# Kernel tuning notes

Hardware: AMD Instinct MI355X
Metric: run time of the kernel (lower is better)

## Reference

```python
import jax, jax.numpy as jnp
import numpy as np
from jax import lax

W = 50      # window size
EPS = 1e-5  # BatchNorm eps (torch default)


def setup_inputs() -> dict:
    key = jax.random.key(0)
    ks = jax.random.split(key, 40)
    def n(i, shape, s=0.1):
        return (jax.random.normal(ks[i], shape, dtype=jnp.float32) * s).astype(jnp.float32)
    inp = {}
    inp['x'] = jax.random.normal(ks[0], (16, 1, 2048), dtype=jnp.float32)
    # conv stack (eval-mode BatchNorm: running mean/var are params)
    inp['conv1_w'] = n(1, (64, 1, 9));  inp['conv1_b'] = n(2, (64,))
    inp['bn1_g'] = 1.0 + n(3, (64,));   inp['bn1_b'] = n(4, (64,))
    inp['bn1_m'] = n(5, (64,));         inp['bn1_v'] = 0.5 + jax.random.uniform(ks[6], (64,), dtype=jnp.float32)
    inp['conv2_w'] = n(7, (32, 64, 7)); inp['conv2_b'] = n(8, (32,))
    inp['bn2_g'] = 1.0 + n(9, (32,));   inp['bn2_b'] = n(10, (32,))
    inp['bn2_m'] = n(11, (32,));        inp['bn2_v'] = 0.5 + jax.random.uniform(ks[12], (32,), dtype=jnp.float32)
    inp['conv3_w'] = n(13, (16, 32, 5)); inp['conv3_b'] = n(14, (16,))
    inp['bn3_g'] = 1.0 + n(15, (16,));   inp['bn3_b'] = n(16, (16,))
    inp['bn3_m'] = n(17, (16,));         inp['bn3_v'] = 0.5 + jax.random.uniform(ks[18], (16,), dtype=jnp.float32)
    # 2-layer LSTM, hidden 64, input 16 (torch gate order i,f,g,o)
    H = 64
    inp['wih0'] = n(19, (4 * H, 16)); inp['whh0'] = n(20, (4 * H, H))
    inp['bih0'] = n(21, (4 * H,));    inp['bhh0'] = n(22, (4 * H,))
    inp['wih1'] = n(23, (4 * H, H));  inp['whh1'] = n(24, (4 * H, H))
    inp['bih1'] = n(25, (4 * H,));    inp['bhh1'] = n(26, (4 * H,))
    # classifier 64 -> 32 -> 2
    inp['fc1_w'] = n(27, (32, H)); inp['fc1_b'] = n(28, (32,))
    inp['fc2_w'] = n(29, (2, 32)); inp['fc2_b'] = n(30, (2,))
    return inp


def _conv1d(x, w, b, pad):
    # x: [N, Cin, L], w: [Cout, Cin, K]
    y = lax.conv_general_dilated(x, w, (1,), [(pad, pad)],
                                 dimension_numbers=('NCH', 'OIH', 'NCH'))
    return y + b[:, None]


def _bn(x, g, b, m, v):
    # eval-mode BatchNorm1d over channel dim of [N, C, L]
    return (x - m[:, None]) * (g / jnp.sqrt(v + EPS))[:, None] + b[:, None]


def _lstm_layer(x, wih, whh, bih, bhh):
    # x: [B, T, D] -> [B, T, H]; torch gate order (i, f, g, o)
    B, T, D = x.shape
    H = whh.shape[1]
    xs = jnp.transpose(x, (1, 0, 2))                     # [T, B, D]
    pre = xs @ wih.T + (bih + bhh)                       # [T, B, 4H] input projection, hoisted
    def step(carry, p):
        h, c = carry
        g = p + h @ whh.T
        i, f, gg, o = jnp.split(g, 4, axis=-1)
        c = jax.nn.sigmoid(f) * c + jax.nn.sigmoid(i) * jnp.tanh(gg)
        h = jax.nn.sigmoid(o) * jnp.tanh(c)
        return (h, c), h
    h0 = jnp.zeros((B, H), x.dtype)
    _, hs = lax.scan(step, (h0, h0), pre)
    return jnp.transpose(hs, (1, 0, 2))


def reference(x, conv1_w, conv1_b, bn1_g, bn1_b, bn1_m, bn1_v,
              conv2_w, conv2_b, bn2_g, bn2_b, bn2_m, bn2_v,
              conv3_w, conv3_b, bn3_g, bn3_b, bn3_m, bn3_v,
              wih0, whh0, bih0, bhh0, wih1, whh1, bih1, bhh1,
              fc1_w, fc1_b, fc2_w, fc2_b):
    B, C, T = x.shape
    # sliding windows with left zero-pad of W-1 -> [B, T, C, W]
    xp = jnp.pad(x, ((0, 0), (0, 0), (W - 1, 0)))
    idx = jnp.arange(T)[:, None] + jnp.arange(W)[None, :]  # [T, W]
    win = xp[:, :, idx]                                    # [B, C, T, W]
    win = jnp.transpose(win, (0, 2, 1, 3)).reshape(B * T, C, W)
    # conv -> BN(eval) -> ReLU stack (dropout is identity in eval)
    h = jax.nn.relu(_bn(_conv1d(win, conv1_w, conv1_b, 4), bn1_g, bn1_b, bn1_m, bn1_v))
    h = jax.nn.relu(_bn(_conv1d(h, conv2_w, conv2_b, 3), bn2_g, bn2_b, bn2_m, bn2_v))
    h = jax.nn.relu(_bn(_conv1d(h, conv3_w, conv3_b, 2), bn3_g, bn3_b, bn3_m, bn3_v))
    feats = h.mean(axis=-1).reshape(B, T, -1)              # AdaptiveAvgPool1d(1) -> [B, T, 16]
    # 2-layer LSTM
    h1 = _lstm_layer(feats, wih0, whh0, bih0, bhh0)
    h2 = _lstm_layer(h1, wih1, whh1, bih1, bhh1)           # [B, T, 64]
    # classifier
    z = jax.nn.relu(h2 @ fc1_w.T + fc1_b)
    logits = z @ fc2_w.T + fc2_b                           # [B, T, 2]
    return logits
```

## Files before the change

kernel.cpp:

```cpp
#include <hip/hip_runtime.h>

#define EPSV 1e-5f
#define SCOPE_AGENT __HIP_MEMORY_SCOPE_AGENT

__device__ __forceinline__ float fast_rcp(float x) { return __builtin_amdgcn_rcpf(x); }
__device__ __forceinline__ float tanhfast(float x) {
    float e = __expf(2.0f * x);
    return 1.0f - 2.0f * fast_rcp(e + 1.0f);
}
__device__ __forceinline__ float dot4(const float4 w, const float4 v, float a) {
    a = fmaf(w.x, v.x, a);
    a = fmaf(w.y, v.y, a);
    a = fmaf(w.z, v.z, a);
    a = fmaf(w.w, v.w, a);
    return a;
}
#define DPPF(v, ctrl) __int_as_float(__builtin_amdgcn_mov_dpp(__float_as_int(v), (ctrl), 0xF, 0xF, false))

typedef unsigned long long ull;

struct RecS {
    float hbuf[2][80];
    float ring[16][64];
    float xst[16][80];
};
struct EdgeS {
    float A1[64 * 40];
    float A2[32 * 32];
    float xeL[24], xeR[24];
    float s1[64], t1[64], s2[32], t2[32], s3[16], t3[16];
    float psumE[288];
    float pi[512];
};

__global__ void pack_kernel(const float* __restrict__ w2, const float* __restrict__ w3,
                            float* __restrict__ w2t2, float4* __restrict__ w3p4,
                            float* __restrict__ w3p1, int* __restrict__ sync_ints) {
    int j = blockIdx.x * 256 + threadIdx.x;
    if (j < 16384) {
        int i = j >> 8;
        int o = (j >> 3) & 31;
        int k = j & 7;
        w2t2[j] = (k < 7) ? w2[o * 448 + i * 7 + k] : 0.0f;
    } else if (j < 16896) {
        int e = j - 16384;
        int i = e >> 4, o = e & 15;
        int base = o * 160 + i * 5;
        w3p4[e] = make_float4(w3[base], w3[base + 1], w3[base + 2], w3[base + 3]);
        w3p1[e] = w3[base + 4];
    } else if (j < 16896 + 4096) {
        sync_ints[j - 16896] = 0;
    }
}

__global__ __launch_bounds__(256) void conv1f_kernel(
    const float* __restrict__ x, const float* __restrict__ w1,
    const float* __restrict__ b1, const float* __restrict__ g1,
    const float* __restrict__ be1, const float* __restrict__ m1,
    const float* __restrict__ vv1, float* __restrict__ a1f)
{
    __shared__ float xs[72];
    const int tid = threadIdx.x;
    const int T = blockIdx.x * 64;
    const int b = blockIdx.y;
    if (tid < 72) {
        int gi = T - 49 + tid;
        xs[tid] = (gi >= 0 && gi < 2048) ? x[b * 2048 + gi] : 0.0f;
    }
    const int i = tid & 63, q = tid >> 6;
    float wv[9];
    #pragma unroll
    for (int k = 0; k < 9; ++k) wv[k] = w1[i * 9 + k];
    float sc = g1[i] * rsqrtf(vv1[i] + EPSV);
    float tc = (b1[i] - m1[i]) * sc + be1[i];
    __syncthreads();
    #pragma unroll
    for (int r = 0; r < 16; ++r) {
        int v1 = T + q * 16 + r;
        if (v1 < 2089) {
            float acc = 0.0f;
            #pragma unroll
            for (int k = 0; k < 9; ++k) acc = fmaf(wv[k], xs[q * 16 + r + k], acc);
            a1f[((long)b * 2089 + v1) * 64 + i] = fmaxf(acc * sc + tc, 0.0f);
        }
    }
}

__global__ __launch_bounds__(256) void conv2f_kernel(
    const float* __restrict__ a1f, const float* __restrict__ w2t2,
    const float* __restrict__ b2, const float* __restrict__ g2,
    const float* __restrict__ be2, const float* __restrict__ m2,
    const float* __restrict__ vv2, float* __restrict__ a2f)
{
    __shared__ __align__(16) float As[64 * 104];
    const int tid = threadIdx.x;
    const int T = blockIdx.x * 64;
    const int b = blockIdx.y;
    for (int idx = tid; idx < 1120; idx += 256) {
        int j = idx >> 4, i4 = (idx & 15) * 4;
        int v1 = T + j; if (v1 > 2088) v1 = 2088;
        float4 f = *(const float4*)&a1f[((long)b * 2089 + v1) * 64 + i4];
        int sj = j + ((j >> 3) << 2);
        As[(i4 + 0) * 104 + sj] = f.x;
        As[(i4 + 1) * 104 + sj] = f.y;
        As[(i4 + 2) * 104 + sj] = f.z;
        As[(i4 + 3) * 104 + sj] = f.w;
    }
    const int o = tid >> 3, pg = tid & 7;
    float sc = g2[o] * rsqrtf(vv2[o] + EPSV);
    float tc = (b2[o] - m2[o]) * sc + be2[o];
    __syncthreads();
    float acc[8];
    #pragma unroll
    for (int q = 0; q < 8; ++q) acc[q] = 0.0f;
    for (int i = 0; i < 64; ++i) {
        const float* rowp = &As[i * 104 + 12 * pg];
        float4 A0 = *(const float4*)&rowp[0];
        float4 A1 = *(const float4*)&rowp[4];
        float4 A2 = *(const float4*)&rowp[12];
        float2 A3 = *(const float2*)&rowp[16];
        const float4* wp = (const float4*)&w2t2[(i * 32 + o) * 8];
        float4 Wa = wp[0], Wb = wp[1];
        float av[14] = {A0.x, A0.y, A0.z, A0.w, A1.x, A1.y, A1.z, A1.w,
                        A2.x, A2.y, A2.z, A2.w, A3.x, A3.y};
        float wk[7] = {Wa.x, Wa.y, Wa.z, Wa.w, Wb.x, Wb.y, Wb.z};
        #pragma unroll
        for (int k = 0; k < 7; ++k) {
            #pragma unroll
            for (int q = 0; q < 8; ++q) acc[q] = fmaf(wk[k], av[q + k], acc[q]);
        }
    }
    #pragma unroll
    for (int q = 0; q < 8; ++q) {
        int v2 = T + pg * 8 + q;
        if (v2 < 2083)
            a2f[((long)b * 2083 + v2) * 32 + o] = fmaxf(acc[q] * sc + tc, 0.0f);
    }
}

__global__ __launch_bounds__(256) void conv3f_kernel(
    const float* __restrict__ a2f,
    const float4* __restrict__ w3p4, const float* __restrict__ w3p1,
    const float* __restrict__ b3, const float* __restrict__ g3,
    const float* __restrict__ be3, const float* __restrict__ m3,
    const float* __restrict__ vv3, float* __restrict__ a3f)
{
    __shared__ __align__(16) float A2s[32 * 200];
    const int tid = threadIdx.x;
    const int T = blockIdx.x * 128;
    const int b = blockIdx.y;
    for (int idx = tid; idx < 1056; idx += 256) {
        int j = idx >> 3, i4 = (idx & 7) * 4;
        int v2 = T + j; if (v2 > 2082) v2 = 2082;
        float4 f = *(const float4*)&a2f[((long)b * 2083 + v2) * 32 + i4];
        int sj = j + ((j >> 3) << 2);
        A2s[(i4 + 0) * 200 + sj] = f.x;
        A2s[(i4 + 1) * 200 + sj] = f.y;
        A2s[(i4 + 2) * 200 + sj] = f.z;
        A2s[(i4 + 3) * 200 + sj] = f.w;
    }
    const int o = tid & 15, pg = tid >> 4;
    float sc = g3[o] * rsqrtf(vv3[o] + EPSV);
    float tc = (b3[o] - m3[o]) * sc + be3[o];
    __syncthreads();
    float acc[8];
    #pragma unroll
    for (int q = 0; q < 8; ++q) acc[q] = 0.0f;
    for (int i = 0; i < 32; ++i) {
        const float* rowp = &A2s[i * 200 + 12 * pg];
        float4 R0 = *(const float4*)&rowp[0];
        float4 R1 = *(const float4*)&rowp[4];
        float4 R2 = *(const float4*)&rowp[12];
        float av[12] = {R0.x, R0.y, R0.z, R0.w, R1.x, R1.y, R1.z, R1.w,
                        R2.x, R2.y, R2.z, R2.w};
        float4 wa = w3p4[i * 16 + o];
        float w4 = w3p1[i * 16 + o];
        #pragma unroll
        for (int q = 0; q < 8; ++q) {
            acc[q] = fmaf(wa.x, av[q], acc[q]);
            acc[q] = fmaf(wa.y, av[q + 1], acc[q]);
            acc[q] = fmaf(wa.z, av[q + 2], acc[q]);
            acc[q] = fmaf(wa.w, av[q + 3], acc[q]);
            acc[q] = fmaf(w4,   av[q + 4], acc[q]);
        }
    }
    #pragma unroll
    for (int q = 0; q < 8; ++q) {
        int v3 = T + pg * 8 + q;
        if (v3 < 2079)
            a3f[((long)b * 2080 + v3) * 16 + o] = fmaxf(acc[q] * sc + tc, 0.0f);
        else if (v3 < 2080)
            a3f[((long)b * 2080 + v3) * 16 + o] = 0.0f;
    }
}

__device__ __forceinline__ void rec0_body(char* smemraw, int b,
    const float* __restrict__ feats,
    const float* __restrict__ wih, const float* __restrict__ whh,
    const float* __restrict__ bih, const float* __restrict__ bhh,
    float* __restrict__ hout, int* __restrict__ cnt0, int* __restrict__ flag1)
{
    RecS* s = (RecS*)smemraw;
    const int tid = threadIdx.x;
    const int j = tid >> 2, kq = tid & 3;

    const float4* pa = (const float4*)(whh + (0 * 64 + j) * 64 + kq * 16);
    const float4* pb = (const float4*)(whh + (1 * 64 + j) * 64 + kq * 16);
    const float4* pc_ = (const float4*)(whh + (2 * 64 + j) * 64 + kq * 16);
    const float4* pd = (const float4*)(whh + (3 * 64 + j) * 64 + kq * 16);
    float4 A0 = pa[0], A1 = pa[1], A2 = pa[2], A3 = pa[3];
    float4 B0 = pb[0], B1 = pb[1], B2 = pb[2], B3 = pb[3];
    float4 C0 = pc_[0], C1 = pc_[1], C2 = pc_[2], C3 = pc_[3];
    float4 D0 = pd[0], D1 = pd[1], D2 = pd[2], D3 = pd[3];
    float4 xw0 = *(const float4*)(wih + (0 * 64 + j) * 16 + kq * 4);
    float4 xw1 = *(const float4*)(wih + (1 * 64 + j) * 16 + kq * 4);
    float4 xw2 = *(const float4*)(wih + (2 * 64 + j) * 16 + kq * 4);
    float4 xw3 = *(const float4*)(wih + (3 * 64 + j) * 16 + kq * 4);
    const float bb0 = bih[j] + bhh[j];
    const float bb1 = bih[64 + j] + bhh[64 + j];
    const float bb2 = bih[128 + j] + bhh[128 + j];
    const float bb3 = bih[192 + j] + bhh[192 + j];

    if (tid < 64) s->hbuf[1][(tid >> 4) * 20 + (tid & 15)] = 0.0f;
    float cst = 0.0f;
    const float* fbase = feats + (long)b * 32768;
    __syncthreads();

#define STEP0(k) { \
        const float4* hp_ = (const float4*)&s->hbuf[((k) + 1) & 1][kq * 20]; \
        float4 h0_ = hp_[0], h1_ = hp_[1], h2_ = hp_[2], h3_ = hp_[3]; \
        float4 xv_ = *(const float4*)&s->xst[(k)][kq * 4]; \
        float p0 = dot4(A3, h3_, dot4(A2, h2_, dot4(A1, h1_, dot4(A0, h0_, dot4(xw0, xv_, 0.f))))); \
        float p1 = dot4(B3, h3_, dot4(B2, h2_, dot4(B1, h1_, dot4(B0, h0_, dot4(xw1, xv_, 0.f))))); \
        float p2 = dot4(C3, h3_, dot4(C2, h2_, dot4(C1, h1_, dot4(C0, h0_, dot4(xw2, xv_, 0.f))))); \
        float p3 = dot4(D3, h3_, dot4(D2, h2_, dot4(D1, h1_, dot4(D0, h0_, dot4(xw3, xv_, 0.f))))); \
        p0 += DPPF(p0, 0xB1); p1 += DPPF(p1, 0xB1); p2 += DPPF(p2, 0xB1); p3 += DPPF(p3, 0xB1); \
        p0 += DPPF(p0, 0x4E); p1 += DPPF(p1, 0x4E); p2 += DPPF(p2, 0x4E); p3 += DPPF(p3, 0x4E); \
        float gi = 1.0f - fast_rcp(__expf(p0 + bb0) + 1.0f); \
        float gf = 1.0f - fast_rcp(__expf(p1 + bb1) + 1.0f); \
        float gg = 1.0f - 2.0f * fast_rcp(__expf(2.0f * (p2 + bb2)) + 1.0f); \
        float go = 1.0f - fast_rcp(__expf(p3 + bb3) + 1.0f); \
        cst = fmaf(gf, cst, gi * gg); \
        float h_ = go * tanhfast(cst); \
        if (kq == 0) { s->hbuf[(k) & 1][(j >> 4) * 20 + (j & 15)] = h_; s->ring[(k)][j] = h_; } \
        __syncthreads(); \
    }

    for (int c = 0; c < 128; ++c) {
        if (tid == 0) {
            while (__hip_atomic_load(&cnt0[b * 128 + c], __ATOMIC_RELAXED, SCOPE_AGENT) < 16)
                __builtin_amdgcn_s_sleep(2);
        }
        __syncthreads();
        s->xst[tid >> 4][tid & 15] =
            __hip_atomic_load(fbase + c * 256 + tid, __ATOMIC_RELAXED, SCOPE_AGENT);
        __syncthreads();
        STEP0(0)  STEP0(1)  STEP0(2)  STEP0(3)
        STEP0(4)  STEP0(5)  STEP0(6)  STEP0(7)
        STEP0(8)  STEP0(9)  STEP0(10) STEP0(11)
        STEP0(12) STEP0(13) STEP0(14) STEP0(15)
        {
            ull* dst = (ull*)(hout + ((long)b * 2048 + c * 16) * 64);
            ull v0 = ((const ull*)s->ring)[tid];
            ull v1 = ((const ull*)s->ring)[tid + 256];
            __hip_atomic_store(dst + tid, v0, __ATOMIC_RELAXED, SCOPE_AGENT);
            __hip_atomic_store(dst + tid + 256, v1, __ATOMIC_RELAXED, SCOPE_AGENT);
            __syncthreads();
            if (tid == 0)
                __hip_atomic_store(&flag1[b * 128 + c], 1, __ATOMIC_RELAXED, SCOPE_AGENT);
        }
    }
#undef STEP0
}

__device__ __forceinline__ void rec1_body(char* smemraw, int b,
    const float* __restrict__ h1o,
    const float* __restrict__ wih, const float* __restrict__ whh,
    const float* __restrict__ bih, const float* __restrict__ bhh,
    float* __restrict__ hout, int* __restrict__ flag1)
{
    RecS* s = (RecS*)smemraw;
    const int tid = threadIdx.x;
    const int j = tid >> 2, kq = tid & 3;

    const float4* pa = (const float4*)(whh + (0 * 64 + j) * 64 + kq * 16);
    const float4* pb = (const float4*)(whh + (1 * 64 + j) * 64 + kq * 16);
    const float4* pc_ = (const float4*)(whh + (2 * 64 + j) * 64 + kq * 16);
    const float4* pd = (const float4*)(whh + (3 * 64 + j) * 64 + kq * 16);
    float4 A0 = pa[0], A1 = pa[1], A2 = pa[2], A3 = pa[3];
    float4 B0 = pb[0], B1 = pb[1], B2 = pb[2], B3 = pb[3];
    float4 C0 = pc_[0], C1 = pc_[1], C2 = pc_[2], C3 = pc_[3];
    float4 D0 = pd[0], D1 = pd[1], D2 = pd[2], D3 = pd[3];
    const float4* qa = (const float4*)(wih + (0 * 64 + j) * 64 + kq * 16);
    const float4* qb = (const float4*)(wih + (1 * 64 + j) * 64 + kq * 16);
    const float4* qc = (const float4*)(wih + (2 * 64 + j) * 64 + kq * 16);
    const float4* qd = (const float4*)(wih + (3 * 64 + j) * 64 + kq * 16);
    float4 XA0 = qa[0], XA1 = qa[1], XA2 = qa[2], XA3 = qa[3];
    float4 XB0 = qb[0], XB1 = qb[1], XB2 = qb[2], XB3 = qb[3];
    float4 XC0 = qc[0], XC1 = qc[1], XC2 = qc[2], XC3 = qc[3];
    float4 XD0 = qd[0], XD1 = qd[1], XD2 = qd[2], XD3 = qd[3];
    const float bb0 = bih[j] + bhh[j];
    const float bb1 = bih[64 + j] + bhh[64 + j];
    const float bb2 = bih[128 + j] + bhh[128 + j];
    const float bb3 = bih[192 + j] + bhh[192 + j];

    if (tid < 64) s->hbuf[1][(tid >> 4) * 20 + (tid & 15)] = 0.0f;
    float cst = 0.0f;
    __syncthreads();

#define STEP1(k) { \
        const float4* hp_ = (const float4*)&s->hbuf[((k) + 1) & 1][kq * 20]; \
        float4 h0_ = hp_[0], h1_ = hp_[1], h2_ = hp_[2], h3_ = hp_[3]; \
        const float4* xp_ = (const float4*)&s->xst[(k)][kq * 20]; \
        float4 x0_ = xp_[0], x1_ = xp_[1], x2_ = xp_[2], x3_ = xp_[3]; \
        float p0 = dot4(A3, h3_, dot4(A2, h2_, dot4(A1, h1_, dot4(A0, h0_, \
                   dot4(XA3, x3_, dot4(XA2, x2_, dot4(XA1, x1_, dot4(XA0, x0_, 0.f)))))))); \
        float p1 = dot4(B3, h3_, dot4(B2, h2_, dot4(B1, h1_, dot4(B0, h0_, \
                   dot4(XB3, x3_, dot4(XB2, x2_, dot4(XB1, x1_, dot4(XB0, x0_, 0.f)))))))); \
        float p2 = dot4(C3, h3_, dot4(C2, h2_, dot4(C1, h1_, dot4(C0, h0_, \
                   dot4(XC3, x3_, dot4(XC2, x2_, dot4(XC1, x1_, dot4(XC0, x0_, 0.f)))))))); \
        float p3 = dot4(D3, h3_, dot4(D2, h2_, dot4(D1, h1_, dot4(D0, h0_, \
                   dot4(XD3, x3_, dot4(XD2, x2_, dot4(XD1, x1_, dot4(XD0, x0_, 0.f)))))))); \
        p0 += DPPF(p0, 0xB1); p1 += DPPF(p1, 0xB1); p2 += DPPF(p2, 0xB1); p3 += DPPF(p3, 0xB1); \
        p0 += DPPF(p0, 0x4E); p1 += DPPF(p1, 0x4E); p2 += DPPF(p2, 0x4E); p3 += DPPF(p3, 0x4E); \
        float gi = 1.0f - fast_rcp(__expf(p0 + bb0) + 1.0f); \
        float gf = 1.0f - fast_rcp(__expf(p1 + bb1) + 1.0f); \
        float gg = 1.0f - 2.0f * fast_rcp(__expf(2.0f * (p2 + bb2)) + 1.0f); \
        float go = 1.0f - fast_rcp(__expf(p3 + bb3) + 1.0f); \
        cst = fmaf(gf, cst, gi * gg); \
        float h_ = go * tanhfast(cst); \
        if (kq == 0) { s->hbuf[(k) & 1][(j >> 4) * 20 + (j & 15)] = h_; s->ring[(k)][j] = h_; } \
        __syncthreads(); \
    }

    for (int c = 0; c < 128; ++c) {
        if (tid == 0) {
            while (__hip_atomic_load(&flag1[b * 128 + c], __ATOMIC_RELAXED, SCOPE_AGENT) < 1)
                __builtin_amdgcn_s_sleep(2);
        }
        __syncthreads();
        {
            const ull* src = (const ull*)(h1o + ((long)b * 2048 + c * 16) * 64);
            ull v0 = __hip_atomic_load(src + tid, __ATOMIC_RELAXED, SCOPE_AGENT);
            ull v1 = __hip_atomic_load(src + tid + 256, __ATOMIC_RELAXED, SCOPE_AGENT);
            int u0 = tid, u1 = tid + 256;
            int k0 = u0 >> 5, p0i = (u0 & 31) * 2;
            int k1 = u1 >> 5, p1i = (u1 & 31) * 2;
            *(ull*)&s->xst[k0][(p0i >> 4) * 20 + (p0i & 15)] = v0;
            *(ull*)&s->xst[k1][(p1i >> 4) * 20 + (p1i & 15)] = v1;
        }
        __syncthreads();
        STEP1(0)  STEP1(1)  STEP1(2)  STEP1(3)
        STEP1(4)  STEP1(5)  STEP1(6)  STEP1(7)
        STEP1(8)  STEP1(9)  STEP1(10) STEP1(11)
        STEP1(12) STEP1(13) STEP1(14) STEP1(15)
        {
            float4* dst = (float4*)(hout + ((long)b * 2048 + c * 16) * 64);
            dst[tid] = ((const float4*)s->ring)[tid];
        }
    }
#undef STEP1
}

__device__ __forceinline__ void edge_body(char* smemraw, int b, int t,
    const float* __restrict__ x,
    const float* __restrict__ w1,
    const float* __restrict__ b1, const float* __restrict__ g1,
    const float* __restrict__ be1, const float* __restrict__ m1, const float* __restrict__ vv1,
    const float* __restrict__ b2, const float* __restrict__ g2,
    const float* __restrict__ be2, const float* __restrict__ m2, const float* __restrict__ vv2,
    const float* __restrict__ b3, const float* __restrict__ g3,
    const float* __restrict__ be3, const float* __restrict__ m3, const float* __restrict__ vv3,
    const float* __restrict__ w2t2,
    const float4* __restrict__ w3p4, const float* __restrict__ w3p1,
    const float* __restrict__ a3f,
    float* __restrict__ feats, int* __restrict__ cnt0)
{
    EdgeS* s = (EdgeS*)smemraw;
    const int tid = threadIdx.x;

    if (tid < 128) {
        int dv = tid >> 2, o4 = (tid & 3) * 4;
        *(float4*)&s->pi[dv * 16 + o4] =
            *(const float4*)&a3f[((long)b * 2080 + t + dv) * 16 + o4];
    }
    if (tid < 64) {
        float sc = g1[tid] * rsqrtf(vv1[tid] + EPSV);
        s->s1[tid] = sc;
        s->t1[tid] = (b1[tid] - m1[tid]) * sc + be1[tid];
    } else if (tid < 96) {
        int o = tid - 64;
        float sc = g2[o] * rsqrtf(vv2[o] + EPSV);
        s->s2[o] = sc;
        s->t2[o] = (b2[o] - m2[o]) * sc + be2[o];
    } else if (tid < 112) {
        int o = tid - 96;
        float sc = g3[o] * rsqrtf(vv3[o] + EPSV);
        s->s3[o] = sc;
        s->t3[o] = (b3[o] - m3[o]) * sc + be3[o];
    } else if (tid < 136) {
        int j = tid - 112;
        float v = 0.0f;
        if (j >= 4 && j < 22) { int gi = t - 53 + j; if (gi >= 0) v = x[b * 2048 + gi]; }
        s->xeL[j] = v;
    } else if (tid < 160) {
        int j = tid - 136;
        float v = 0.0f;
        if (j <= 17) { int gi = t - 17 + j; if (gi >= 0) v = x[b * 2048 + gi]; }
        s->xeR[j] = v;
    }
    for (int idx = tid; idx < 384; idx += 256) {
        int o = idx / 6, z = idx - o * 6;
        s->A1[o * 40 + (z < 3 ? z : 31 + z)] = 0.0f;
    }
    if (tid < 128) {
        int o = tid >> 2, z = tid & 3;
        s->A2[o * 32 + (z < 2 ? z : 25 + z)] = 0.0f;
    }
    __syncthreads();

    {
        int o = tid >> 2, g = tid & 3;
        float wv[9];
        #pragma unroll
        for (int k = 0; k < 9; ++k) wv[k] = w1[o * 9 + k];
        float sc = s->s1[o], tc = s->t1[o];
        #pragma unroll
        for (int n = 0; n < 7; ++n) {
            int P = g * 7 + n;
            float acc = 0.0f;
            if (P < 14) {
                #pragma unroll
                for (int k = 0; k < 9; ++k) acc = fmaf(wv[k], s->xeL[P + k], acc);
                s->A1[o * 40 + 3 + P] = fmaxf(acc * sc + tc, 0.0f);
            } else {
                int pr = P - 14;
                #pragma unroll
                for (int k = 0; k < 9; ++k) acc = fmaf(wv[k], s->xeR[pr + k], acc);
                s->A1[o * 40 + 20 + pr] = fmaxf(acc * sc + tc, 0.0f);
            }
        }
    }
    __syncthreads();

    {
        int o = tid >> 3, g = tid & 7;
        int side = g >> 2, gg = g & 3;
        int be_ = gg * 3;
        int cnt = (gg == 3) ? 2 : 3;
        int beta0 = side ? 20 + be_ : be_;
        float acc0 = 0.f, acc1 = 0.f, acc2 = 0.f;
        for (int i = 0; i < 64; ++i) {
            const float* rp = &s->A1[i * 40 + beta0];
            float av[9];
            #pragma unroll
            for (int c = 0; c < 9; ++c) av[c] = rp[c];
            const float4* wp = (const float4*)&w2t2[(i * 32 + o) * 8];
            float4 Wa = wp[0], Wb = wp[1];
            float wk[7] = {Wa.x, Wa.y, Wa.z, Wa.w, Wb.x, Wb.y, Wb.z};
            #pragma unroll
            for (int k = 0; k < 7; ++k) {
                acc0 = fmaf(wk[k], av[k], acc0);
                acc1 = fmaf(wk[k], av[k + 1], acc1);
                acc2 = fmaf(wk[k], av[k + 2], acc2);
            }
        }
        float sc = s->s2[o], tc = s->t2[o];
        float r0 = fmaxf(acc0 * sc + tc, 0.0f);
        float r1 = fmaxf(acc1 * sc + tc, 0.0f);
        float r2 = fmaxf(acc2 * sc + tc, 0.0f);
        int base = o * 32 + (side ? 16 + be_ : 2 + be_);
        s->A2[base] = r0;
        s->A2[base + 1] = r1;
        if (cnt == 3) s->A2[base + 2] = r2;
    }
    __syncthreads();

    {
        int o = tid & 15, g = tid >> 4;
        float sc = s->s3[o], tc = s->t3[o];
        #pragma unroll
        for (int rep = 0; rep < 2; ++rep) {
            int P3 = (rep == 0) ? g : 16 + g;
            if (rep == 1 && g >= 2) break;
            int tb = (P3 >= 9) ? 16 + (P3 - 9) : P3;
            float acc = 0.0f;
            for (int i = 0; i < 32; ++i) {
                const float* rp = &s->A2[i * 32 + tb];
                float4 wa = w3p4[i * 16 + o];
                float w4 = w3p1[i * 16 + o];
                acc = fmaf(wa.x, rp[0], acc);
                acc = fmaf(wa.y, rp[1], acc);
                acc = fmaf(wa.z, rp[2], acc);
                acc = fmaf(wa.w, rp[3], acc);
                acc = fmaf(w4,   rp[4], acc);
            }
            s->psumE[P3 * 16 + o] = fmaxf(acc * sc + tc, 0.0f);
        }
    }
    __syncthreads();

    if (tid < 16) {
        float e = 0.0f;
        #pragma unroll
        for (int P3 = 0; P3 < 18; ++P3) e += s->psumE[P3 * 16 + tid];
        float ii = 0.0f;
        #pragma unroll
        for (int dv = 0; dv < 32; ++dv) ii += s->pi[dv * 16 + tid];
        __hip_atomic_store(&feats[((long)b * 2048 + t) * 16 + tid], (e + ii) * (1.0f / 50.0f),
                           __ATOMIC_RELAXED, SCOPE_AGENT);
    }
    __syncthreads();
    if (tid == 0)
        __hip_atomic_fetch_add(&cnt0[b * 128 + (t >> 4)], 1, __ATOMIC_RELAXED, SCOPE_AGENT);
}

__global__ __launch_bounds__(256, 2) void fused_kernel(
    const float* __restrict__ x,
    const float* __restrict__ w1, const float* __restrict__ b1,
    const float* __restrict__ g1, const float* __restrict__ be1,
    const float* __restrict__ m1, const float* __restrict__ vv1,
    const float* __restrict__ b2,
    const float* __restrict__ g2, const float* __restrict__ be2,
    const float* __restrict__ m2, const float* __restrict__ vv2,
    const float* __restrict__ b3,
    const float* __restrict__ g3, const float* __restrict__ be3,
    const float* __restrict__ m3, const float* __restrict__ vv3,
    const float* __restrict__ w2t2,
    const float4* __restrict__ w3p4, const float* __restrict__ w3p1,
    const float* __restrict__ a3f,
    const float* __restrict__ wih0, const float* __restrict__ whh0,
    const float* __restrict__ bih0, const float* __restrict__ bhh0,
    const float* __restrict__ wih1, const float* __restrict__ whh1,
    const float* __restrict__ bih1, const float* __restrict__ bhh1,
    float* __restrict__ feats, float* __restrict__ h1o, float* __restrict__ h2o,
    int* __restrict__ cnt0, int* __restrict__ flag1)
{
    __shared__ __align__(16) char smem[sizeof(EdgeS) > sizeof(RecS) ? sizeof(EdgeS) : sizeof(RecS)];

    if (blockIdx.x < 16) { rec0_body(smem, blockIdx.x, feats, wih0, whh0, bih0, bhh0, h1o, cnt0, flag1); return; }
    if (blockIdx.x < 32) { rec1_body(smem, blockIdx.x - 16, h1o, wih1, whh1, bih1, bhh1, h2o, flag1); return; }

    int w = blockIdx.x - 32;
    int b = w & 15;
    int t = w >> 4;
    edge_body(smem, b, t, x, w1, b1, g1, be1, m1, vv1, b2, g2, be2, m2, vv2,
              b3, g3, be3, m3, vv3, w2t2, w3p4, w3p1, a3f, feats, cnt0);
}

__global__ __launch_bounds__(256) void fc_kernel(
    const float* __restrict__ h2o,
    const float* __restrict__ fc1w, const float* __restrict__ fc1b,
    const float* __restrict__ fc2w, const float* __restrict__ fc2b,
    float* __restrict__ out)
{
    int r = blockIdx.x * 256 + threadIdx.x;
    float h[64];
    const float4* hp = (const float4*)(h2o + (long)r * 64);
    #pragma unroll
    for (int i = 0; i < 16; ++i) {
        float4 v = hp[i];
        h[4 * i] = v.x; h[4 * i + 1] = v.y; h[4 * i + 2] = v.z; h[4 * i + 3] = v.w;
    }
    float l0 = fc2b[0], l1 = fc2b[1];
    #pragma unroll 4
    for (int j = 0; j < 32; ++j) {
        float z = fc1b[j];
        #pragma unroll
        for (int k = 0; k < 64; ++k) z = fmaf(h[k], fc1w[j * 64 + k], z);
        z = fmaxf(z, 0.0f);
        l0 = fmaf(z, fc2w[j], l0);
        l1 = fmaf(z, fc2w[32 + j], l1);
    }
    out[r * 2] = l0;
    out[r * 2 + 1] = l1;
}

extern "C" void kernel_launch(void* const* d_in, const int* in_sizes, int n_in,
                              void* d_out, int out_size, void* d_ws, size_t ws_size,
                              hipStream_t stream) {
    const float* x    = (const float*)d_in[0];
    const float* w1   = (const float*)d_in[1];
    const float* b1   = (const float*)d_in[2];
    const float* g1   = (const float*)d_in[3];
    const float* be1  = (const float*)d_in[4];
    const float* m1   = (const float*)d_in[5];
    const float* v1   = (const float*)d_in[6];
    const float* w2   = (const float*)d_in[7];
    const float* b2   = (const float*)d_in[8];
    const float* g2   = (const float*)d_in[9];
    const float* be2  = (const float*)d_in[10];
    const float* m2   = (const float*)d_in[11];
    const float* v2   = (const float*)d_in[12];
    const float* w3   = (const float*)d_in[13];
    const float* b3   = (const float*)d_in[14];
    const float* g3   = (const float*)d_in[15];
    const float* be3  = (const float*)d_in[16];
    const float* m3   = (const float*)d_in[17];
    const float* v3   = (const float*)d_in[18];
    const float* wih0 = (const float*)d_in[19];
    const float* whh0 = (const float*)d_in[20];
    const float* bih0 = (const float*)d_in[21];
    const float* bhh0 = (const float*)d_in[22];
    const float* wih1 = (const float*)d_in[23];
    const float* whh1 = (const float*)d_in[24];
    const float* bih1 = (const float*)d_in[25];
    const float* bhh1 = (const float*)d_in[26];
    const float* fc1w = (const float*)d_in[27];
    const float* fc1b = (const float*)d_in[28];
    const float* fc2w = (const float*)d_in[29];
    const float* fc2b = (const float*)d_in[30];
    float* out = (float*)d_out;

    float* ws    = (float*)d_ws;
    float* feats = ws;
    float* h2o   = feats + 32768 * 16;
    float* w2t2  = h2o + 32768 * 64;
    float* w3p4f = w2t2 + 16384;
    float* w3p1  = w3p4f + 2048;
    float* h1o   = w3p1 + 512;
    float* a1f   = h1o + 32768 * 64;
    float* a2f   = a1f + 16 * 2089 * 64;
    float* a3f   = a2f + 16 * 2083 * 32;
    int*   cnt0  = (int*)(a3f + 16 * 2080 * 16);
    int*   flag1 = cnt0 + 2048;

    hipLaunchKernelGGL(pack_kernel, dim3(82), dim3(256), 0, stream,
                       w2, w3, w2t2, (float4*)w3p4f, w3p1, cnt0);
    hipLaunchKernelGGL(conv1f_kernel, dim3(33, 16), dim3(256), 0, stream,
                       x, w1, b1, g1, be1, m1, v1, a1f);
    hipLaunchKernelGGL(conv2f_kernel, dim3(33, 16), dim3(256), 0, stream,
                       a1f, w2t2, b2, g2, be2, m2, v2, a2f);
    hipLaunchKernelGGL(conv3f_kernel, dim3(17, 16), dim3(256), 0, stream,
                       a2f, (const float4*)w3p4f, w3p1, b3, g3, be3, m3, v3, a3f);
    hipLaunchKernelGGL(fused_kernel, dim3(32 + 32768), dim3(256), 0, stream,
                       x, w1, b1, g1, be1, m1, v1, b2, g2, be2, m2, v2,
                       b3, g3, be3, m3, v3, w2t2, (const float4*)w3p4f, w3p1, a3f,
                       wih0, whh0, bih0, bhh0, wih1, whh1, bih1, bhh1,
                       feats, h1o, h2o, cnt0, flag1);
    hipLaunchKernelGGL(fc_kernel, dim3(128), dim3(256), 0, stream,
                       h2o, fc1w, fc1b, fc2w, fc2b, out);
}
```

Before: 1.203 ms.

## Reuse precomputed interior conv activations in edge windows and split channel reductions

New measurement: 1.687 ms. 40.3% more time.

```diff
diff --git a/kernel.cpp b/kernel.cpp
--- a/kernel.cpp
+++ b/kernel.cpp
@@ -25,9 +25,9 @@
     float xst[16][80];
 };
 struct EdgeS {
-    float A1[64 * 40];
-    float A2[32 * 32];
-    float xeL[24], xeR[24];
+    float A1[64 * 36];
+    float A2[32 * 36];
+    float xl[16], xr[16];
     float s1[64], t1[64], s2[32], t2[32], s3[16], t3[16];
     float psumE[288];
     float pi[512];
@@ -373,12 +373,25 @@
     const float* __restrict__ be3, const float* __restrict__ m3, const float* __restrict__ vv3,
     const float* __restrict__ w2t2,
     const float4* __restrict__ w3p4, const float* __restrict__ w3p1,
+    const float* __restrict__ a1f, const float* __restrict__ a2f,
     const float* __restrict__ a3f,
     float* __restrict__ feats, int* __restrict__ cnt0)
 {
     EdgeS* s = (EdgeS*)smemraw;
     const int tid = threadIdx.x;
 
+    for (int idx = tid; idx < 1088; idx += 256) {
+        if (idx < 768) {
+            int row = idx / 12, z = idx - row * 12;
+            int slot = (z < 3) ? z : (z < 6 ? 10 + z : 20 + z);
+            s->A1[row * 36 + slot] = 0.0f;
+        } else {
+            int e = idx - 768;
+            int row = e / 10, z = e - row * 10;
+            int slot = (z < 2) ? z : (z < 5 ? 11 + z : 22 + z);
+            s->A2[row * 36 + slot] = 0.0f;
+        }
+    }
     if (tid < 128) {
         int dv = tid >> 2, o4 = (tid & 3) * 4;
         *(float4*)&s->pi[dv * 16 + o4] =
@@ -398,104 +411,159 @@
         float sc = g3[o] * rsqrtf(vv3[o] + EPSV);
         s->s3[o] = sc;
         s->t3[o] = (b3[o] - m3[o]) * sc + be3[o];
-    } else if (tid < 136) {
-        int j = tid - 112;
+    } else if (tid < 128) {
+        int m = tid - 112;
         float v = 0.0f;
-        if (j >= 4 && j < 22) { int gi = t - 53 + j; if (gi >= 0) v = x[b * 2048 + gi]; }
-        s->xeL[j] = v;
-    } else if (tid < 160) {
-        int j = tid - 136;
+        if (m >= 4) { int gi = t - 53 + m; if (gi >= 0) v = x[b * 2048 + gi]; }
+        s->xl[m] = v;
+    } else if (tid < 144) {
+        int m = tid - 128;
         float v = 0.0f;
-        if (j <= 17) { int gi = t - 17 + j; if (gi >= 0) v = x[b * 2048 + gi]; }
-        s->xeR[j] = v;
-    }
-    for (int idx = tid; idx < 384; idx += 256) {
-        int o = idx / 6, z = idx - o * 6;
-        s->A1[o * 40 + (z < 3 ? z : 31 + z)] = 0.0f;
-    }
-    if (tid < 128) {
-        int o = tid >> 2, z = tid & 3;
-        s->A2[o * 32 + (z < 2 ? z : 25 + z)] = 0.0f;
-    }
-    __syncthreads();
-
+        if (m <= 7) { int gi = t - 7 + m; if (gi >= 0) v = x[b * 2048 + gi]; }
+        s->xr[m] = v;
+    }
     {
-        int o = tid >> 2, g = tid & 3;
+        if (tid < 96) {
+            int d = tid >> 4, i4 = (tid & 15) * 4;
+            float4 f = *(const float4*)&a1f[((long)b * 2089 + t + d) * 64 + i4];
+            int slot = 7 + d;
+            s->A1[(i4 + 0) * 36 + slot] = f.x;
+            s->A1[(i4 + 1) * 36 + slot] = f.y;
+            s->A1[(i4 + 2) * 36 + slot] = f.z;
+            s->A1[(i4 + 3) * 36 + slot] = f.w;
+        } else if (tid < 192) {
+            int e = tid - 96;
+            int d = e >> 4, i4 = (e & 15) * 4;
+            float4 f = *(const float4*)&a1f[((long)b * 2089 + t + 36 + d) * 64 + i4];
+            int slot = 16 + d;
+            s->A1[(i4 + 0) * 36 + slot] = f.x;
+            s->A1[(i4 + 1) * 36 + slot] = f.y;
+            s->A1[(i4 + 2) * 36 + slot] = f.z;
+            s->A1[(i4 + 3) * 36 + slot] = f.w;
+        } else if (tid < 224) {
+            int e = tid - 192;
+            int d = e >> 3, i4 = (e & 7) * 4;
+            float4 f = *(const float4*)&a2f[((long)b * 2083 + t + d) * 32 + i4];
+            int slot = 9 + d;
+            s->A2[(i4 + 0) * 36 + slot] = f.x;
+            s->A2[(i4 + 1) * 36 + slot] = f.y;
+            s->A2[(i4 + 2) * 36 + slot] = f.z;
+            s->A2[(i4 + 3) * 36 + slot] = f.w;
+        } else {
+            int e = tid - 224;
+            int d = e >> 3, i4 = (e & 7) * 4;
+            float4 f = *(const float4*)&a2f[((long)b * 2083 + t + 32 + d) * 32 + i4];
+            int slot = 16 + d;
+            s->A2[(i4 + 0) * 36 + slot] = f.x;
+            s->A2[(i4 + 1) * 36 + slot] = f.y;
+            s->A2[(i4 + 2) * 36 + slot] = f.z;
+            s->A2[(i4 + 3) * 36 + slot] = f.w;
+        }
+    }
+    __syncthreads();
+
+    {
+        const int o = tid >> 2, g = tid & 3;
         float wv[9];
         #pragma unroll
         for (int k = 0; k < 9; ++k) wv[k] = w1[o * 9 + k];
+        float accL = 0.0f, accR = 0.0f;
+        #pragma unroll
+        for (int k = 0; k < 9; ++k) {
+            accL = fmaf(wv[k], s->xl[g + k], accL);
+            accR = fmaf(wv[k], s->xr[g + k], accR);
+        }
         float sc = s->s1[o], tc = s->t1[o];
-        #pragma unroll
-        for (int n = 0; n < 7; ++n) {
-            int P = g * 7 + n;
-            float acc = 0.0f;
-            if (P < 14) {
-                #pragma unroll
-                for (int k = 0; k < 9; ++k) acc = fmaf(wv[k], s->xeL[P + k], acc);
-                s->A1[o * 40 + 3 + P] = fmaxf(acc * sc + tc, 0.0f);
-            } else {
-                int pr = P - 14;
-                #pragma unroll
-                for (int k = 0; k < 9; ++k) acc = fmaf(wv[k], s->xeR[pr + k], acc);
-                s->A1[o * 40 + 20 + pr] = fmaxf(acc * sc + tc, 0.0f);
-            }
-        }
+        s->A1[o * 36 + 3 + g]  = fmaxf(accL * sc + tc, 0.0f);
+        s->A1[o * 36 + 22 + g] = fmaxf(accR * sc + tc, 0.0f);
     }
     __syncthreads();
 
     {
-        int o = tid >> 3, g = tid & 7;
-        int side = g >> 2, gg = g & 3;
-        int be_ = gg * 3;
-        int cnt = (gg == 3) ? 2 : 3;
-        int beta0 = side ? 20 + be_ : be_;
-        float acc0 = 0.f, acc1 = 0.f, acc2 = 0.f;
-        for (int i = 0; i < 64; ++i) {
-            const float* rp = &s->A1[i * 40 + beta0];
-            float av[9];
-            #pragma unroll
-            for (int c = 0; c < 9; ++c) av[c] = rp[c];
+        const int o = tid >> 3, side = (tid >> 2) & 1, isub = tid & 3;
+        const int sbase = side * 16;
+        float acc[7];
+        #pragma unroll
+        for (int q = 0; q < 7; ++q) acc[q] = 0.0f;
+        #pragma unroll 2
+        for (int ii = 0; ii < 16; ++ii) {
+            int i = 4 * ii + isub;
+            const float* rp = &s->A1[i * 36 + sbase];
+            float4 R0 = *(const float4*)&rp[0];
+            float4 R1 = *(const float4*)&rp[4];
+            float4 R2 = *(const float4*)&rp[8];
+            float r12 = rp[12];
+            float av[13] = {R0.x, R0.y, R0.z, R0.w, R1.x, R1.y, R1.z, R1.w,
+                            R2.x, R2.y, R2.z, R2.w, r12};
             const float4* wp = (const float4*)&w2t2[(i * 32 + o) * 8];
             float4 Wa = wp[0], Wb = wp[1];
             float wk[7] = {Wa.x, Wa.y, Wa.z, Wa.w, Wb.x, Wb.y, Wb.z};
             #pragma unroll
             for (int k = 0; k < 7; ++k) {
-                acc0 = fmaf(wk[k], av[k], acc0);
-                acc1 = fmaf(wk[k], av[k + 1], acc1);
-                acc2 = fmaf(wk[k], av[k + 2], acc2);
+                #pragma unroll
+                for (int q = 0; q < 7; ++q) acc[q] = fmaf(wk[k], av[q + k], acc[q]);
             }
         }
-        float sc = s->s2[o], tc = s->t2[o];
-        float r0 = fmaxf(acc0 * sc + tc, 0.0f);
-        float r1 = fmaxf(acc1 * sc + tc, 0.0f);
-        float r2 = fmaxf(acc2 * sc + tc, 0.0f);
-        int base = o * 32 + (side ? 16 + be_ : 2 + be_);
-        s->A2[base] = r0;
-        s->A2[base + 1] = r1;
-        if (cnt == 3) s->A2[base + 2] = r2;
+        #pragma unroll
+        for (int q = 0; q < 7; ++q) {
+            acc[q] += DPPF(acc[q], 0xB1);
+            acc[q] += DPPF(acc[q], 0x4E);
+        }
+        if (isub == 0) {
+            float sc = s->s2[o], tc = s->t2[o];
+            #pragma unroll
+            for (int q = 0; q < 7; ++q) {
+                float r = fmaxf(acc[q] * sc + tc, 0.0f);
+                s->A2[o * 36 + (side ? 20 + q : 2 + q)] = r;
+            }
+        }
     }
     __syncthreads();
 
     {
-        int o = tid & 15, g = tid >> 4;
-        float sc = s->s3[o], tc = s->t3[o];
-        #pragma unroll
-        for (int rep = 0; rep < 2; ++rep) {
-            int P3 = (rep == 0) ? g : 16 + g;
-            if (rep == 1 && g >= 2) break;
-            int tb = (P3 >= 9) ? 16 + (P3 - 9) : P3;
-            float acc = 0.0f;
-            for (int i = 0; i < 32; ++i) {
-                const float* rp = &s->A2[i * 32 + tb];
-                float4 wa = w3p4[i * 16 + o];
-                float w4 = w3p1[i * 16 + o];
-                acc = fmaf(wa.x, rp[0], acc);
-                acc = fmaf(wa.y, rp[1], acc);
-                acc = fmaf(wa.z, rp[2], acc);
-                acc = fmaf(wa.w, rp[3], acc);
-                acc = fmaf(w4,   rp[4], acc);
+        const int o = (tid >> 2) & 15, isub = tid & 3;
+        const int side = (tid >> 6) & 1, pg = tid >> 7;
+        const int p0n = pg * 5;
+        float acc[5];
+        #pragma unroll
+        for (int n = 0; n < 5; ++n) acc[n] = 0.0f;
+        #pragma unroll 2
+        for (int ii = 0; ii < 8; ++ii) {
+            int i = 4 * ii + isub;
+            const float* rp = &s->A2[i * 36 + side * 16];
+            float4 R0 = *(const float4*)&rp[0];
+            float4 R1 = *(const float4*)&rp[4];
+            float4 R2 = *(const float4*)&rp[8];
+            float r12 = rp[12];
+            float av[13] = {R0.x, R0.y, R0.z, R0.w, R1.x, R1.y, R1.z, R1.w,
+                            R2.x, R2.y, R2.z, R2.w, r12};
+            float4 wa = w3p4[i * 16 + o];
+            float w4 = w3p1[i * 16 + o];
+            #pragma unroll
+            for (int n = 0; n < 5; ++n) {
+                int P = p0n + n;
+                if (P < 9) {
+                    acc[n] = fmaf(wa.x, av[P], acc[n]);
+                    acc[n] = fmaf(wa.y, av[P + 1], acc[n]);
+                    acc[n] = fmaf(wa.z, av[P + 2], acc[n]);
+                    acc[n] = fmaf(wa.w, av[P + 3], acc[n]);
+                    acc[n] = fmaf(w4,   av[P + 4], acc[n]);
+                }
             }
-            s->psumE[P3 * 16 + o] = fmaxf(acc * sc + tc, 0.0f);
+        }
+        #pragma unroll
+        for (int n = 0; n < 5; ++n) {
+            acc[n] += DPPF(acc[n], 0xB1);
+            acc[n] += DPPF(acc[n], 0x4E);
+        }
+        if (isub == 0) {
+            float sc = s->s3[o], tc = s->t3[o];
+            #pragma unroll
+            for (int n = 0; n < 5; ++n) {
+                int P = p0n + n;
+                if (P < 9)
+                    s->psumE[(side * 9 + P) * 16 + o] = fmaxf(acc[n] * sc + tc, 0.0f);
+            }
         }
     }
     __syncthreads();
@@ -528,6 +596,7 @@
     const float* __restrict__ m3, const float* __restrict__ vv3,
     const float* __restrict__ w2t2,
     const float4* __restrict__ w3p4, const float* __restrict__ w3p1,
+    const float* __restrict__ a1f, const float* __restrict__ a2f,
     const float* __restrict__ a3f,
     const float* __restrict__ wih0, const float* __restrict__ whh0,
     const float* __restrict__ bih0, const float* __restrict__ bhh0,
@@ -545,7 +614,7 @@
     int b = w & 15;
     int t = w >> 4;
     edge_body(smem, b, t, x, w1, b1, g1, be1, m1, vv1, b2, g2, be2, m2, vv2,
-              b3, g3, be3, m3, vv3, w2t2, w3p4, w3p1, a3f, feats, cnt0);
+              b3, g3, be3, m3, vv3, w2t2, w3p4, w3p1, a1f, a2f, a3f, feats, cnt0);
 }
 
 __global__ __launch_bounds__(256) void fc_kernel(
@@ -635,7 +704,8 @@
                        a2f, (const float4*)w3p4f, w3p1, b3, g3, be3, m3, v3, a3f);
     hipLaunchKernelGGL(fused_kernel, dim3(32 + 32768), dim3(256), 0, stream,
                        x, w1, b1, g1, be1, m1, v1, b2, g2, be2, m2, v2,
-                       b3, g3, be3, m3, v3, w2t2, (const float4*)w3p4f, w3p1, a3f,
+                       b3, g3, be3, m3, v3, w2t2, (const float4*)w3p4f, w3p1,
+                       a1f, a2f, a3f,
                        wih0, whh0, bih0, bhh0, wih1, whh1, bih1, bhh1,
                        feats, h1o, h2o, cnt0, flag1);
     hipLaunchKernelGGL(fc_kernel, dim3(128), dim3(256), 0, stream,
```
